# Performance work log

Hardware: AMD Instinct MI355X
Metric: run time of the kernel (lower is better)

The kernel has to match this reference:

```python
import jax, jax.numpy as jnp
import numpy as np

HIDDEN = 2048
NUM_HEADS = 16
HEAD_DIM = 128
INNER = NUM_HEADS * HEAD_DIM
ROPE_BASE = 10000.0


def apply_rope(x):
    # x: [B, H, S, D], rotate-half (NeoX-style) RoPE
    B, H, S, D = x.shape
    inv_freq = 1.0 / (ROPE_BASE ** (jnp.arange(0, D, 2, dtype=jnp.float32) / D))
    t = jnp.arange(S, dtype=jnp.float32)
    freqs = t[:, None] * inv_freq[None, :]          # [S, D/2]
    cos = jnp.concatenate([jnp.cos(freqs)] * 2, -1)  # [S, D]
    sin = jnp.concatenate([jnp.sin(freqs)] * 2, -1)
    x1, x2 = x[..., : D // 2], x[..., D // 2:]
    rotated = jnp.concatenate([-x2, x1], axis=-1)
    return x * cos[None, None] + rotated * sin[None, None]


def setup_inputs() -> dict:
    key = jax.random.key(0)
    ks = jax.random.split(key, 9)
    s = 1.0 / np.sqrt(HIDDEN)
    return {
        "hidden_states": jax.random.normal(ks[0], (2, 2048, HIDDEN), jnp.float32),
        "Wq": jax.random.uniform(ks[1], (INNER, HIDDEN), jnp.float32, -s, s),
        "bq": jax.random.uniform(ks[2], (INNER,), jnp.float32, -s, s),
        "Wk": jax.random.uniform(ks[3], (INNER, HIDDEN), jnp.float32, -s, s),
        "bk": jax.random.uniform(ks[4], (INNER,), jnp.float32, -s, s),
        "Wv": jax.random.uniform(ks[5], (INNER, HIDDEN), jnp.float32, -s, s),
        "bv": jax.random.uniform(ks[6], (INNER,), jnp.float32, -s, s),
        "Wo": jax.random.uniform(ks[7], (HIDDEN, INNER), jnp.float32, -s, s),
        "bo": jax.random.uniform(ks[8], (HIDDEN,), jnp.float32, -s, s),
    }


def reference(hidden_states, Wq, bq, Wk, bk, Wv, bv, Wo, bo):
    B, S, _ = hidden_states.shape

    def heads(x):  # [B,S,inner] -> [B,H,S,D]
        return x.reshape(B, S, NUM_HEADS, HEAD_DIM).transpose(0, 2, 1, 3)

    q = heads(hidden_states @ Wq.T + bq)
    k = heads(hidden_states @ Wk.T + bk)
    v = heads(hidden_states @ Wv.T + bv)
    q = apply_rope(q)
    k = apply_rope(k)

    scores = jnp.einsum("bhqd,bhkd->bhqk", q, k) / jnp.sqrt(
        jnp.asarray(HEAD_DIM, q.dtype))
    causal = jnp.tril(jnp.ones((S, S), dtype=bool))
    scores = jnp.where(causal[None, None], scores, jnp.finfo(scores.dtype).min)
    weights = jax.nn.softmax(scores, axis=-1)
    context = jnp.einsum("bhqk,bhkd->bhqd", weights, v)
    merged = context.transpose(0, 2, 1, 3).reshape(B, S, INNER)
    return merged @ Wo.T + bo
```

## Files before the change

### kernel.cpp

```cpp
#include <hip/hip_runtime.h>

using u16 = unsigned short;
using u32 = unsigned int;

typedef __attribute__((ext_vector_type(4))) float f32x4;
typedef __attribute__((ext_vector_type(8))) short frag8;

#define HIDDEN 2048
#define SEQ    2048
#define NHEADS 16
#define HDIM   128

__device__ __forceinline__ float bf2f(u16 u) {
  union { u32 i; float f; } c; c.i = ((u32)u) << 16; return c.f;
}
__device__ __forceinline__ u16 f2bf(float f) {
  union { float f; u32 i; } c; c.f = f;
  u32 u = c.i + 0x7fffu + ((c.i >> 16) & 1u);
  return (u16)(u >> 16);
}

__global__ void cvt_all(const float* __restrict__ X,
                        const float* __restrict__ W0, const float* __restrict__ W1,
                        const float* __restrict__ W2, const float* __restrict__ W3,
                        u16* __restrict__ dX,
                        u16* __restrict__ dW0, u16* __restrict__ dW1,
                        u16* __restrict__ dW2, u16* __restrict__ dW3)
{
  const int bx = blockIdx.x;
  const float* s; u16* d; int g;
  if (bx < 4096) { s = X; d = dX; g = bx * 256 + threadIdx.x; }
  else {
    const int t = bx - 4096;
    const int w = t >> 11;
    s = (w == 0) ? W0 : (w == 1) ? W1 : (w == 2) ? W2 : W3;
    d = (w == 0) ? dW0 : (w == 1) ? dW1 : (w == 2) ? dW2 : dW3;
    g = (t & 2047) * 256 + threadIdx.x;
  }
  const float* p = s + (size_t)g * 8;
  f32x4 x0 = *(const f32x4*)p, x1 = *(const f32x4*)(p + 4);
  frag8 o;
#pragma unroll
  for (int e = 0; e < 4; e++) { o[e] = (short)f2bf(x0[e]); o[e+4] = (short)f2bf(x1[e]); }
  *(frag8*)(d + (size_t)g * 8) = o;
}

template<int W_BF16, int NW, int VT, int C_F32>
__global__ __launch_bounds__(256, 4)
void gemm_fused(const u16* __restrict__ A,
                const void* __restrict__ W0, const void* __restrict__ W1,
                const void* __restrict__ W2,
                const float* __restrict__ bias0, const float* __restrict__ bias1,
                const float* __restrict__ bias2,
                void* __restrict__ C0, void* __restrict__ C1, void* __restrict__ C2)
{
  __shared__ __align__(16) u16 smem[8192];
  u16* As = smem;
  u16* Bs = smem + 4096;

  const int tid  = threadIdx.x;
  const int lane = tid & 63;
  const int wv   = tid >> 6;
  const int quad = lane >> 4;
  const int l16  = lane & 15;
  const int wm = wv >> 1, wn = wv & 1;
  const int m0 = blockIdx.y * 128;
  const int wix = (NW == 1) ? 0 : (blockIdx.x >> 4);
  const int n0  = ((NW == 1) ? blockIdx.x : (blockIdx.x & 15)) * 128;

  const void* Wp = (wix == 0) ? W0 : (wix == 1) ? W1 : W2;
  const float* bias = (wix == 0) ? bias0 : (wix == 1) ? bias1 : bias2;
  void* Cp = (wix == 0) ? C0 : (wix == 1) ? C1 : C2;

  f32x4 acc[4][4];
#pragma unroll
  for (int i = 0; i < 4; i++)
#pragma unroll
    for (int j = 0; j < 4; j++) acc[i][j] = (f32x4)0.0f;

  const int g0 = tid, g1 = tid + 256;
  const int r0 = g0 >> 2, c0 = (g0 & 3) * 8;
  const int r1 = g1 >> 2, c1 = (g1 & 3) * 8;

  for (int k0 = 0; k0 < HIDDEN; k0 += 32) {
    __builtin_amdgcn_global_load_lds(
      (const __attribute__((address_space(1))) void*)(A + (size_t)(m0 + r0) * HIDDEN + k0 + c0),
      (__attribute__((address_space(3))) void*)(As + g0 * 8), 16, 0, 0);
    __builtin_amdgcn_global_load_lds(
      (const __attribute__((address_space(1))) void*)(A + (size_t)(m0 + r1) * HIDDEN + k0 + c1),
      (__attribute__((address_space(3))) void*)(As + g1 * 8), 16, 0, 0);
    if (W_BF16) {
      const u16* Wb = (const u16*)Wp;
      __builtin_amdgcn_global_load_lds(
        (const __attribute__((address_space(1))) void*)(Wb + (size_t)(n0 + r0) * HIDDEN + k0 + c0),
        (__attribute__((address_space(3))) void*)(Bs + g0 * 8), 16, 0, 0);
      __builtin_amdgcn_global_load_lds(
        (const __attribute__((address_space(1))) void*)(Wb + (size_t)(n0 + r1) * HIDDEN + k0 + c1),
        (__attribute__((address_space(3))) void*)(Bs + g1 * 8), 16, 0, 0);
    } else {
      const float* Wf = (const float*)Wp;
      const float* p0 = Wf + (size_t)(n0 + r0) * HIDDEN + k0 + c0;
      const float* p1 = Wf + (size_t)(n0 + r1) * HIDDEN + k0 + c1;
      f32x4 x0 = *(const f32x4*)p0, x1 = *(const f32x4*)(p0 + 4);
      f32x4 y0 = *(const f32x4*)p1, y1 = *(const f32x4*)(p1 + 4);
      frag8 b0v, b1v;
#pragma unroll
      for (int e = 0; e < 4; e++) {
        b0v[e]   = (short)f2bf(x0[e]); b0v[e+4] = (short)f2bf(x1[e]);
        b1v[e]   = (short)f2bf(y0[e]); b1v[e+4] = (short)f2bf(y1[e]);
      }
      *(frag8*)&Bs[g0 * 8] = b0v;
      *(frag8*)&Bs[g1 * 8] = b1v;
    }

    __builtin_amdgcn_s_waitcnt(0);
    __syncthreads();

    frag8 af[4], bfr[4];
#pragma unroll
    for (int mt = 0; mt < 4; mt++)
      af[mt] = *(const frag8*)&As[(wm*64 + mt*16 + l16) * 32 + quad*8];
#pragma unroll
    for (int nt = 0; nt < 4; nt++)
      bfr[nt] = *(const frag8*)&Bs[(wn*64 + nt*16 + l16) * 32 + quad*8];
#pragma unroll
    for (int mt = 0; mt < 4; mt++)
#pragma unroll
      for (int nt = 0; nt < 4; nt++)
        acc[mt][nt] = __builtin_amdgcn_mfma_f32_16x16x32_bf16(af[mt], bfr[nt], acc[mt][nt], 0, 0, 0);

    __syncthreads();
  }

  if (VT && wix == 2) {
    u16* Cv = (u16*)Cp;
    u16* T = smem + wv * 1056;
#pragma unroll
    for (int nt = 0; nt < 4; nt++) {
      const int n  = n0 + wn*64 + nt*16 + l16;
      const float bv = bias[n];
#pragma unroll
      for (int mt = 0; mt < 4; mt++)
#pragma unroll
        for (int r = 0; r < 4; r++)
          T[l16 * 66 + mt*16 + quad*4 + r] = f2bf(acc[mt][nt][r] + bv);
#pragma unroll
      for (int rr = 0; rr < 16; rr++) {
        const int nn = n0 + wn*64 + nt*16 + rr;
        const int mm = m0 + wm*64 + lane;
        const int b = mm >> 11, s = mm & 2047;
        Cv[((size_t)(b * HIDDEN + nn)) * SEQ + s] = T[rr * 66 + lane];
      }
    }
  } else {
#pragma unroll
    for (int nt = 0; nt < 4; nt++) {
      const int n  = n0 + wn*64 + nt*16 + l16;
      const float bv = bias[n];
#pragma unroll
      for (int mt = 0; mt < 4; mt++) {
#pragma unroll
        for (int r = 0; r < 4; r++) {
          const int m = m0 + wm*64 + mt*16 + quad*4 + r;
          if (C_F32) ((float*)Cp)[(size_t)m * HIDDEN + n] = acc[mt][nt][r] + bv;
          else       ((u16*)Cp)[(size_t)m * HIDDEN + n]   = f2bf(acc[mt][nt][r] + bv);
        }
      }
    }
  }
}

#define NT32 32

#define STG(gptr, lofs) __builtin_amdgcn_global_load_lds( \
    (const __attribute__((address_space(1))) void*)(gptr), \
    (__attribute__((address_space(3))) void*)(smem + (lofs)), 16, 0, 0)

#define GRP(t, DOSTAGE, WAITSTR) { \
  u16* As = smem + ((t) % 3) * 24576; \
  u16* Bs = As + 16384; \
  frag8 af[8], bfr[2]; \
  _Pragma("unroll") for (int mt = 0; mt < 8; mt++) \
    af[mt] = *(const frag8*)(As + abase + mt*1024 + s0q); \
  bfr[0] = *(const frag8*)(Bs + bbase + s0q); \
  bfr[1] = *(const frag8*)(Bs + bbase + 1024 + s0q); \
  if (DOSTAGE) { \
    const size_t ko = (size_t)((t)+2)*64; const int sb = (((t)+2)%3)*24576; \
    STG(gA0 + ko, sb + ldsA0); STG(gA1 + ko, sb + ldsA1); STG(gB0 + ko, sb + ldsB0); \
  } \
  __builtin_amdgcn_s_barrier(); \
  __builtin_amdgcn_s_setprio(1); \
  _Pragma("unroll") for (int mt = 0; mt < 8; mt++) { \
    acc[mt][0] = __builtin_amdgcn_mfma_f32_16x16x32_bf16(af[mt], bfr[0], acc[mt][0], 0,0,0); \
    acc[mt][1] = __builtin_amdgcn_mfma_f32_16x16x32_bf16(af[mt], bfr[1], acc[mt][1], 0,0,0); \
  } \
  __builtin_amdgcn_s_setprio(0); \
  __builtin_amdgcn_s_barrier(); \
  _Pragma("unroll") for (int mt = 0; mt < 8; mt++) \
    af[mt] = *(const frag8*)(As + abase + mt*1024 + s1q); \
  bfr[0] = *(const frag8*)(Bs + bbase + s1q); \
  bfr[1] = *(const frag8*)(Bs + bbase + 1024 + s1q); \
  if (DOSTAGE) { \
    const size_t ko = (size_t)((t)+2)*64; const int sb = (((t)+2)%3)*24576; \
    STG(gA2 + ko, sb + ldsA2); STG(gA3 + ko, sb + ldsA3); STG(gB1 + ko, sb + ldsB1); \
  } \
  __builtin_amdgcn_s_barrier(); \
  __builtin_amdgcn_s_setprio(1); \
  _Pragma("unroll") for (int mt = 0; mt < 8; mt++) { \
    acc[mt][0] = __builtin_amdgcn_mfma_f32_16x16x32_bf16(af[mt], bfr[0], acc[mt][0], 0,0,0); \
    acc[mt][1] = __builtin_amdgcn_mfma_f32_16x16x32_bf16(af[mt], bfr[1], acc[mt][1], 0,0,0); \
  } \
  __builtin_amdgcn_s_setprio(0); \
  asm volatile("s_waitcnt " WAITSTR ::: "memory"); \
  __builtin_amdgcn_s_barrier(); \
}

#define G256_SETUP(Abase, Wbase) \
  const int tid  = threadIdx.x; \
  const int lane = tid & 63; \
  const int wv   = tid >> 6; \
  const int quad = lane >> 4; \
  const int l16  = lane & 15; \
  const int wm = wv >> 2, wn = wv & 3; \
  const int c8 = (lane & 7) ^ (lane >> 3); \
  const int rA = lane >> 3; \
  const u16* gA0 = (Abase) + (size_t)(m0 + wv*32 +  0 + rA) * HIDDEN + c8*8; \
  const u16* gA1 = (Abase) + (size_t)(m0 + wv*32 +  8 + rA) * HIDDEN + c8*8; \
  const u16* gA2 = (Abase) + (size_t)(m0 + wv*32 + 16 + rA) * HIDDEN + c8*8; \
  const u16* gA3 = (Abase) + (size_t)(m0 + wv*32 + 24 + rA) * HIDDEN + c8*8; \
  const u16* gB0 = (Wbase) + (size_t)(n0 + wv*16 +  0 + rA) * HIDDEN + c8*8; \
  const u16* gB1 = (Wbase) + (size_t)(n0 + wv*16 +  8 + rA) * HIDDEN + c8*8; \
  const int ldsA0 = (4*wv)*512 + lane*8; \
  const int ldsA1 = ldsA0 + 512; \
  const int ldsA2 = ldsA0 + 1024; \
  const int ldsA3 = ldsA0 + 1536; \
  const int ldsB0 = 16384 + (2*wv)*512 + lane*8; \
  const int ldsB1 = ldsB0 + 512; \
  const int s0q = ((quad    ) ^ (l16 & 7)) * 8; \
  const int s1q = ((quad + 4) ^ (l16 & 7)) * 8; \
  const int abase = (wm*128 + l16) * 64; \
  const int bbase = (wn*32  + l16) * 64; \
  f32x4 acc[8][2]; \
  _Pragma("unroll") \
  for (int i = 0; i < 8; i++) { acc[i][0] = (f32x4)0.0f; acc[i][1] = (f32x4)0.0f; } \
  STG(gA0, ldsA0); STG(gA1, ldsA1); STG(gB0, ldsB0); \
  STG(gA2, ldsA2); STG(gA3, ldsA3); STG(gB1, ldsB1); \
  STG(gA0 + 64, 24576 + ldsA0); STG(gA1 + 64, 24576 + ldsA1); STG(gB0 + 64, 24576 + ldsB0); \
  STG(gA2 + 64, 24576 + ldsA2); STG(gA3 + 64, 24576 + ldsA3); STG(gB1 + 64, 24576 + ldsB1); \
  asm volatile("s_waitcnt vmcnt(6)" ::: "memory"); \
  __builtin_amdgcn_s_barrier(); \
  for (int t = 0; t < NT32 - 2; ++t) GRP(t, 1, "vmcnt(6)"); \
  GRP(NT32 - 2, 0, "vmcnt(0)"); \
  GRP(NT32 - 1, 0, "vmcnt(63)");

__global__ __launch_bounds__(512, 2)
void gemm256_qkv(const u16* __restrict__ A,
                 const u16* __restrict__ W0, const u16* __restrict__ W1,
                 const u16* __restrict__ W2,
                 const float* __restrict__ bias0, const float* __restrict__ bias1,
                 const float* __restrict__ bias2,
                 u16* __restrict__ C0, u16* __restrict__ C1, u16* __restrict__ Vt)
{
  __shared__ __align__(16) u16 smem[73728];

  const int bid = blockIdx.x;
  const int sbid = (bid & 7) * 96 + (bid >> 3);
  const int colTile = sbid >> 4;
  const int rowTile = sbid & 15;
  const int wix = colTile >> 4;
  const int n0  = (colTile & 15) * 128;
  const int m0  = rowTile * 256;

  const u16* Wp = (wix == 0) ? W0 : (wix == 1) ? W1 : W2;
  const float* bias = (wix == 0) ? bias0 : (wix == 1) ? bias1 : bias2;

  G256_SETUP(A, Wp)

  if (wix != 2) {
    u16* Cb = (wix == 0) ? C0 : C1;
#pragma unroll
    for (int nt = 0; nt < 2; nt++) {
      const int n = n0 + wn*32 + nt*16 + l16;
      const float bv = bias[n];
#pragma unroll
      for (int mt = 0; mt < 8; mt++) {
        const int m = m0 + wm*128 + mt*16 + quad*4;
#pragma unroll
        for (int r = 0; r < 4; r++)
          Cb[(size_t)(m + r) * HIDDEN + n] = f2bf(acc[mt][nt][r] + bv);
      }
    }
  } else {
    u16* T = smem + wv * 2176;
    const int b  = m0 >> 11;
    const int s0 = (m0 & 2047) + wm*128;
#pragma unroll
    for (int nt = 0; nt < 2; nt++) {
      const int nloc = n0 + wn*32 + nt*16;
      const float bv = bias[nloc + l16];
#pragma unroll
      for (int mt = 0; mt < 8; mt++)
#pragma unroll
        for (int r = 0; r < 4; r++)
          T[l16*136 + mt*16 + quad*4 + r] = f2bf(acc[mt][nt][r] + bv);
#pragma unroll
      for (int rr = 0; rr < 16; rr++) {
        const size_t vb = ((size_t)(b * HIDDEN + nloc + rr)) * SEQ + s0;
        Vt[vb + lane]      = T[rr*136 + lane];
        Vt[vb + 64 + lane] = T[rr*136 + 64 + lane];
      }
    }
  }
}

__global__ __launch_bounds__(512, 2)
void gemm256_o(const u16* __restrict__ A, const u16* __restrict__ W,
               const float* __restrict__ bias, float* __restrict__ C)
{
  __shared__ __align__(16) u16 smem[73728];

  const int bid = blockIdx.x;
  const int sbid = (bid & 7) * 32 + (bid >> 3);
  const int colTile = sbid >> 4;
  const int rowTile = sbid & 15;
  const int n0  = colTile * 128;
  const int m0  = rowTile * 256;

  G256_SETUP(A, W)

#pragma unroll
  for (int nt = 0; nt < 2; nt++) {
    const int n = n0 + wn*32 + nt*16 + l16;
    const float bv = bias[n];
#pragma unroll
    for (int mt = 0; mt < 8; mt++) {
      const int m = m0 + wm*128 + mt*16 + quad*4;
#pragma unroll
      for (int r = 0; r < 4; r++)
        C[(size_t)(m + r) * HIDDEN + n] = acc[mt][nt][r] + bv;
    }
  }
}

__global__ void rope_kernel(u16* __restrict__ Q, u16* __restrict__ K)
{
  const int tid = blockIdx.x * 256 + threadIdx.x;
  const int t   = tid >> 19;
  const int r   = tid & 524287;
  const int row = r >> 7;
  const int grp = r & 127;
  const int h   = grp >> 3, d0 = (grp & 7) * 8;
  u16* X = t ? K : Q;
  const float s = (float)(row & 2047);
  const float qscale = t ? 1.0f : 0.08838834764831845f;
  const size_t base = (size_t)row * HIDDEN + h * HDIM + d0;
  frag8 a = *(const frag8*)(X + base);
  frag8 b = *(const frag8*)(X + base + 64);
  frag8 oa, ob;
#pragma unroll
  for (int e = 0; e < 8; e++) {
    const float inv = __expf(-(float)(d0 + e) * (9.210340371976184f / 64.0f));
    float sn, c;
    __sincosf(s * inv, &sn, &c);
    const float x1 = bf2f((u16)a[e]), x2 = bf2f((u16)b[e]);
    oa[e] = (short)f2bf((x1 * c - x2 * sn) * qscale);
    ob[e] = (short)f2bf((x2 * c + x1 * sn) * qscale);
  }
  *(frag8*)(X + base)      = oa;
  *(frag8*)(X + base + 64) = ob;
}

#define PS_STR 68
__global__ __launch_bounds__(256, 2)
void attn_kernel(const u16* Q, const u16* __restrict__ K,
                 const u16* __restrict__ Vt, u16* O)
{
  __shared__ __align__(16) u16 smem[25088];

  const int bx = blockIdx.x;
  const int g  = bx >> 5;
  const int bh = bx & 31;
  const int qt = (g & 1) ? (15 - (g >> 1)) : (g >> 1);
  const int b = bh >> 4, h = bh & 15;

  const int tid = threadIdx.x, lane = tid & 63, wv = tid >> 6;
  const int quad = lane >> 4, l16 = lane & 15;
  const int l7 = l16 & 7;

  const size_t krow0 = (size_t)(b * SEQ) * HIDDEN + h * HDIM;
  const size_t vrow0 = (size_t)(b * HIDDEN + h * HDIM) * SEQ;

  frag8 qf[2][4];
  const size_t qbase = ((size_t)(b * SEQ) + qt*128 + wv*32) * HIDDEN + h * HDIM;
#pragma unroll
  for (int mq = 0; mq < 2; mq++)
#pragma unroll
    for (int ks = 0; ks < 4; ks++)
      qf[mq][ks] = *(const frag8*)(Q + qbase + (size_t)(mq*16 + l16) * HIDDEN + ks*32 + quad*8);

  const int kr4 = lane >> 4, kc = lane & 15;
  const int vr8 = lane >> 3;
  const u16* gK[4]; const u16* gV[4];
  int ldsK[4], ldsV[4];
#pragma unroll
  for (int it = 0; it < 4; it++) {
    const int kcs = kc ^ ((it*4 + kr4) & 7);
    gK[it] = K + krow0 + (size_t)(wv*16 + it*4 + kr4) * HIDDEN + kcs*8;
    ldsK[it] = (wv*16 + it*4)*128 + lane*8;
    const int vcs = (lane & 7) ^ vr8;
    gV[it] = Vt + vrow0 + (size_t)(wv*32 + it*8 + vr8) * SEQ + vcs*8;
    ldsV[it] = 8192 + (wv*32 + it*8)*64 + lane*8;
  }

  f32x4 Oacc[2][8];
#pragma unroll
  for (int mq = 0; mq < 2; mq++)
#pragma unroll
    for (int dt = 0; dt < 8; dt++) Oacc[mq][dt] = (f32x4)0.0f;
  float m_i[2][4], l_i[2][4];
#pragma unroll
  for (int mq = 0; mq < 2; mq++)
#pragma unroll
    for (int r = 0; r < 4; r++) { m_i[mq][r] = -1e30f; l_i[mq][r] = 0.0f; }

  const int ktmax = 2*qt + 2;
  u16* Pp = smem + 16384 + wv*2176;

  for (int kt = 0; kt < ktmax; kt++) {
#pragma unroll
    for (int it = 0; it < 4; it++) {
      __builtin_amdgcn_global_load_lds(
        (const __attribute__((address_space(1))) void*)(gK[it] + (size_t)kt*64*HIDDEN),
        (__attribute__((address_space(3))) void*)(smem + ldsK[it]), 16, 0, 0);
      __builtin_amdgcn_global_load_lds(
        (const __attribute__((address_space(1))) void*)(gV[it] + kt*64),
        (__attribute__((address_space(3))) void*)(smem + ldsV[it]), 16, 0, 0);
    }
    asm volatile("s_waitcnt vmcnt(0)" ::: "memory");
    __syncthreads();

    f32x4 st[2][4];
#pragma unroll
    for (int mq = 0; mq < 2; mq++)
#pragma unroll
      for (int jt = 0; jt < 4; jt++) st[mq][jt] = (f32x4)0.0f;

    __builtin_amdgcn_s_setprio(1);
#pragma unroll
    for (int ks = 0; ks < 4; ks++) {
      frag8 kf[4];
#pragma unroll
      for (int jt = 0; jt < 4; jt++)
        kf[jt] = *(const frag8*)&smem[(jt*16 + l16)*128 + (((ks*4+quad) ^ l7))*8];
#pragma unroll
      for (int jt = 0; jt < 4; jt++) {
        st[0][jt] = __builtin_amdgcn_mfma_f32_16x16x32_bf16(qf[0][ks], kf[jt], st[0][jt], 0, 0, 0);
        st[1][jt] = __builtin_amdgcn_mfma_f32_16x16x32_bf16(qf[1][ks], kf[jt], st[1][jt], 0, 0, 0);
      }
    }
    __builtin_amdgcn_s_setprio(0);

    if (kt >= 2*qt) {
#pragma unroll
      for (int mq = 0; mq < 2; mq++)
#pragma unroll
        for (int jt = 0; jt < 4; jt++) {
          const int jl = kt*64 + jt*16 + l16;
#pragma unroll
          for (int r = 0; r < 4; r++) {
            const int ml = qt*128 + wv*32 + mq*16 + quad*4 + r;
            st[mq][jt][r] = (jl <= ml) ? st[mq][jt][r] : -1e30f;
          }
        }
    }

    float alpha[2][4];
    int needresc = 0;
#pragma unroll
    for (int mq = 0; mq < 2; mq++)
#pragma unroll
      for (int r = 0; r < 4; r++) {
        float cm = fmaxf(fmaxf(st[mq][0][r], st[mq][1][r]),
                         fmaxf(st[mq][2][r], st[mq][3][r]));
        cm = fmaxf(cm, __shfl_xor(cm, 1, 64));
        cm = fmaxf(cm, __shfl_xor(cm, 2, 64));
        cm = fmaxf(cm, __shfl_xor(cm, 4, 64));
        cm = fmaxf(cm, __shfl_xor(cm, 8, 64));
        if (cm > m_i[mq][r] + 8.0f) {
          alpha[mq][r] = __expf(m_i[mq][r] - cm);
          m_i[mq][r] = cm;
          needresc = 1;
        } else {
          alpha[mq][r] = 1.0f;
        }
      }

#pragma unroll
    for (int mq = 0; mq < 2; mq++) {
      float csum[4];
#pragma unroll
      for (int r = 0; r < 4; r++) csum[r] = 0.0f;
#pragma unroll
      for (int jt = 0; jt < 4; jt++)
#pragma unroll
        for (int r = 0; r < 4; r++) {
          const float p = __expf(st[mq][jt][r] - m_i[mq][r]);
          csum[r] += p;
          Pp[mq*1088 + (quad*4 + r) * PS_STR + jt*16 + l16] = f2bf(p);
        }
#pragma unroll
      for (int r = 0; r < 4; r++) {
        float cs = csum[r];
        cs += __shfl_xor(cs, 1, 64);
        cs += __shfl_xor(cs, 2, 64);
        cs += __shfl_xor(cs, 4, 64);
        cs += __shfl_xor(cs, 8, 64);
        l_i[mq][r] = l_i[mq][r] * alpha[mq][r] + cs;
      }
    }
    if (__any(needresc)) {
#pragma unroll
      for (int mq = 0; mq < 2; mq++)
#pragma unroll
        for (int r = 0; r < 4; r++)
#pragma unroll
          for (int dt = 0; dt < 8; dt++) Oacc[mq][dt][r] *= alpha[mq][r];
    }

    __builtin_amdgcn_s_setprio(1);
#pragma unroll
    for (int ks2 = 0; ks2 < 2; ks2++) {
      frag8 pf0 = *(const frag8*)&Pp[l16 * PS_STR + ks2*32 + quad*8];
      frag8 pf1 = *(const frag8*)&Pp[1088 + l16 * PS_STR + ks2*32 + quad*8];
#pragma unroll
      for (int dt = 0; dt < 8; dt++) {
        frag8 vf = *(const frag8*)&smem[8192 + (dt*16 + l16)*64 + ((ks2*4+quad) ^ l7)*8];
        Oacc[0][dt] = __builtin_amdgcn_mfma_f32_16x16x32_bf16(pf0, vf, Oacc[0][dt], 0, 0, 0);
        Oacc[1][dt] = __builtin_amdgcn_mfma_f32_16x16x32_bf16(pf1, vf, Oacc[1][dt], 0, 0, 0);
      }
    }
    __builtin_amdgcn_s_setprio(0);
    __syncthreads();
  }

#pragma unroll
  for (int mq = 0; mq < 2; mq++)
#pragma unroll
    for (int r = 0; r < 4; r++) {
      const float inv = 1.0f / l_i[mq][r];
      const int m = qt*128 + wv*32 + mq*16 + quad*4 + r;
#pragma unroll
      for (int dt = 0; dt < 8; dt++) {
        const int d = dt*16 + l16;
        O[((size_t)(b * SEQ) + m) * HIDDEN + h * HDIM + d] = f2bf(Oacc[mq][dt][r] * inv);
      }
    }
}

extern "C" void kernel_launch(void* const* d_in, const int* in_sizes, int n_in,
                              void* d_out, int out_size, void* d_ws, size_t ws_size,
                              hipStream_t stream)
{
  const float* X  = (const float*)d_in[0];
  const float* Wq = (const float*)d_in[1];
  const float* bq = (const float*)d_in[2];
  const float* Wk = (const float*)d_in[3];
  const float* bk = (const float*)d_in[4];
  const float* Wv = (const float*)d_in[5];
  const float* bv = (const float*)d_in[6];
  const float* Wo = (const float*)d_in[7];
  const float* bo = (const float*)d_in[8];
  float* out = (float*)d_out;

  u16* Kb = (u16*)d_out;
  u16* Xb = (u16*)d_out + (8u << 20);
  char* ws = (char*)d_ws;
  u16* Qb  = (u16*)ws;
  u16* Vtb = (u16*)(ws + (16u << 20));

  dim3 blk(256);
  const bool fast = ws_size >= (64u << 20);
  if (fast) {
    u16* Wqb = (u16*)(ws + (32u << 20));
    u16* Wkb = (u16*)(ws + (40u << 20));
    u16* Wvb = (u16*)(ws + (48u << 20));
    u16* Wob = (u16*)(ws + (56u << 20));
    cvt_all<<<12288, blk, 0, stream>>>(X, Wq, Wk, Wv, Wo, Xb, Wqb, Wkb, Wvb, Wob);
    gemm256_qkv<<<dim3(768), dim3(512), 0, stream>>>(
        Xb, Wqb, Wkb, Wvb, bq, bk, bv, Qb, Kb, Vtb);
    rope_kernel<<<4096, blk, 0, stream>>>(Qb, Kb);
    attn_kernel<<<512, blk, 0, stream>>>(Qb, Kb, Vtb, Qb);
    gemm256_o<<<dim3(256), dim3(512), 0, stream>>>(Qb, Wob, bo, out);
  } else {
    cvt_all<<<4096, blk, 0, stream>>>(X, Wq, Wk, Wv, Wo, Xb, Xb, Xb, Xb, Xb);
    gemm_fused<0,3,1,0><<<dim3(48,32), blk, 0, stream>>>(
        Xb, Wq, Wk, Wv, bq, bk, bv, Qb, Kb, Vtb);
    rope_kernel<<<4096, blk, 0, stream>>>(Qb, Kb);
    attn_kernel<<<512, blk, 0, stream>>>(Qb, Kb, Vtb, Qb);
    gemm_fused<0,1,0,1><<<dim3(16,32), blk, 0, stream>>>(
        Qb, Wo, Wo, Wo, bo, bo, bo, out, out, out);
  }
}
```

Before: 430.3 us.

## Double-buffer K/V tiles in LDS and process query subtiles sequentially

Splits the shared K and V tiles into two LDS buffers. The global-to-LDS load of the next key tile is issued before computing on the current one, which removes the per-iteration vmcnt(0) stall. To fit the extra buffers, the per-wave P staging area is halved, and the two 16-row query subtiles now run softmax and PV one after another, reusing that buffer. LDS per block grows to about 74 KB, and correctness now relies on the barrier waiting for the outstanding LDS DMA writes.

```diff
diff --git a/kernel.cpp b/kernel.cpp
--- a/kernel.cpp
+++ b/kernel.cpp
@@ -371,11 +371,23 @@
 }
 
 #define PS_STR 68
+
+#define ATT_STAGE(kt_, bufsel) { \
+  const size_t ko_ = (size_t)(kt_) * 64; \
+  _Pragma("unroll") for (int it = 0; it < 4; it++) { \
+    __builtin_amdgcn_global_load_lds( \
+      (const __attribute__((address_space(1))) void*)(gK[it] + ko_ * HIDDEN), \
+      (__attribute__((address_space(3))) void*)(smem + (bufsel)*8192 + ldsK[it]), 16, 0, 0); \
+    __builtin_amdgcn_global_load_lds( \
+      (const __attribute__((address_space(1))) void*)(gV[it] + ko_), \
+      (__attribute__((address_space(3))) void*)(smem + 16384 + (bufsel)*8192 + ldsV[it]), 16, 0, 0); \
+  } }
+
 __global__ __launch_bounds__(256, 2)
 void attn_kernel(const u16* Q, const u16* __restrict__ K,
                  const u16* __restrict__ Vt, u16* O)
 {
-  __shared__ __align__(16) u16 smem[25088];
+  __shared__ __align__(16) u16 smem[37120];
 
   const int bx = blockIdx.x;
   const int g  = bx >> 5;
@@ -409,7 +421,7 @@
     ldsK[it] = (wv*16 + it*4)*128 + lane*8;
     const int vcs = (lane & 7) ^ vr8;
     gV[it] = Vt + vrow0 + (size_t)(wv*32 + it*8 + vr8) * SEQ + vcs*8;
-    ldsV[it] = 8192 + (wv*32 + it*8)*64 + lane*8;
+    ldsV[it] = (wv*32 + it*8)*64 + lane*8;
   }
 
   f32x4 Oacc[2][8];
@@ -424,20 +436,17 @@
     for (int r = 0; r < 4; r++) { m_i[mq][r] = -1e30f; l_i[mq][r] = 0.0f; }
 
   const int ktmax = 2*qt + 2;
-  u16* Pp = smem + 16384 + wv*2176;
+  u16* Pp = smem + 32768 + wv*1088;
+
+  ATT_STAGE(0, 0)
+  __syncthreads();
 
   for (int kt = 0; kt < ktmax; kt++) {
-#pragma unroll
-    for (int it = 0; it < 4; it++) {
-      __builtin_amdgcn_global_load_lds(
-        (const __attribute__((address_space(1))) void*)(gK[it] + (size_t)kt*64*HIDDEN),
-        (__attribute__((address_space(3))) void*)(smem + ldsK[it]), 16, 0, 0);
-      __builtin_amdgcn_global_load_lds(
-        (const __attribute__((address_space(1))) void*)(gV[it] + kt*64),
-        (__attribute__((address_space(3))) void*)(smem + ldsV[it]), 16, 0, 0);
-    }
-    asm volatile("s_waitcnt vmcnt(0)" ::: "memory");
-    __syncthreads();
+    const int cb = kt & 1;
+    if (kt + 1 < ktmax) ATT_STAGE(kt + 1, cb ^ 1)
+
+    const u16* Kb_ = smem + cb*8192;
+    const u16* Vb_ = smem + 16384 + cb*8192;
 
     f32x4 st[2][4];
 #pragma unroll
@@ -451,7 +460,7 @@
       frag8 kf[4];
 #pragma unroll
       for (int jt = 0; jt < 4; jt++)
-        kf[jt] = *(const frag8*)&smem[(jt*16 + l16)*128 + (((ks*4+quad) ^ l7))*8];
+        kf[jt] = *(const frag8*)&Kb_[(jt*16 + l16)*128 + ((ks*4 + quad) ^ l7)*8];
 #pragma unroll
       for (int jt = 0; jt < 4; jt++) {
         st[0][jt] = __builtin_amdgcn_mfma_f32_16x16x32_bf16(qf[0][ks], kf[jt], st[0][jt], 0, 0, 0);
@@ -494,6 +503,7 @@
           alpha[mq][r] = 1.0f;
         }
       }
+    const int resc = __any(needresc);
 
 #pragma unroll
     for (int mq = 0; mq < 2; mq++) {
@@ -506,7 +516,7 @@
         for (int r = 0; r < 4; r++) {
           const float p = __expf(st[mq][jt][r] - m_i[mq][r]);
           csum[r] += p;
-          Pp[mq*1088 + (quad*4 + r) * PS_STR + jt*16 + l16] = f2bf(p);
+          Pp[(quad*4 + r) * PS_STR + jt*16 + l16] = f2bf(p);
         }
 #pragma unroll
       for (int r = 0; r < 4; r++) {
@@ -517,29 +527,26 @@
         cs += __shfl_xor(cs, 8, 64);
         l_i[mq][r] = l_i[mq][r] * alpha[mq][r] + cs;
       }
-    }
-    if (__any(needresc)) {
-#pragma unroll
-      for (int mq = 0; mq < 2; mq++)
+      if (resc) {
 #pragma unroll
         for (int r = 0; r < 4; r++)
 #pragma unroll
           for (int dt = 0; dt < 8; dt++) Oacc[mq][dt][r] *= alpha[mq][r];
-    }
-
-    __builtin_amdgcn_s_setprio(1);
-#pragma unroll
-    for (int ks2 = 0; ks2 < 2; ks2++) {
-      frag8 pf0 = *(const frag8*)&Pp[l16 * PS_STR + ks2*32 + quad*8];
-      frag8 pf1 = *(const frag8*)&Pp[1088 + l16 * PS_STR + ks2*32 + quad*8];
-#pragma unroll
-      for (int dt = 0; dt < 8; dt++) {
-        frag8 vf = *(const frag8*)&smem[8192 + (dt*16 + l16)*64 + ((ks2*4+quad) ^ l7)*8];
-        Oacc[0][dt] = __builtin_amdgcn_mfma_f32_16x16x32_bf16(pf0, vf, Oacc[0][dt], 0, 0, 0);
-        Oacc[1][dt] = __builtin_amdgcn_mfma_f32_16x16x32_bf16(pf1, vf, Oacc[1][dt], 0, 0, 0);
-      }
-    }
-    __builtin_amdgcn_s_setprio(0);
+      }
+
+      __builtin_amdgcn_s_setprio(1);
+#pragma unroll
+      for (int ks2 = 0; ks2 < 2; ks2++) {
+        frag8 pf = *(const frag8*)&Pp[l16 * PS_STR + ks2*32 + quad*8];
+#pragma unroll
+        for (int dt = 0; dt < 8; dt++) {
+          frag8 vf = *(const frag8*)&Vb_[(dt*16 + l16)*64 + ((ks2*4 + quad) ^ l7)*8];
+          Oacc[mq][dt] = __builtin_amdgcn_mfma_f32_16x16x32_bf16(pf, vf, Oacc[mq][dt], 0, 0, 0);
+        }
+      }
+      __builtin_amdgcn_s_setprio(0);
+    }
+
     __syncthreads();
   }
 
```

New measurement: 440.9 us. 2.5% more time.
